# Kernel tuning notes

Hardware: AMD Instinct MI355X
Metric: run time of the kernel (lower is better)

The kernel has to match this reference:

```python
import jax, jax.numpy as jnp
import numpy as np

GROUPS = 8
EPS = 1e-3  # Keras GroupNormalization default epsilon


def group_norm(x, gamma, beta):
    b, h, w, c = x.shape
    xr = x.reshape(b, h, w, GROUPS, c // GROUPS)
    mean = jnp.mean(xr, axis=(1, 2, 4), keepdims=True)
    var = jnp.var(xr, axis=(1, 2, 4), keepdims=True)
    xn = ((xr - mean) * jax.lax.rsqrt(var + EPS)).reshape(b, h, w, c)
    return xn * gamma + beta


def setup_inputs() -> dict:
    key = jax.random.key(0)
    ks = jax.random.split(key, 6)
    B, H, W, C = 4, 64, 64, 256
    std = C ** -0.5
    return {
        "x": jax.random.normal(ks[0], (B, H, W, C), dtype=jnp.float32),
        "gamma": jnp.ones((C,), jnp.float32),
        "beta": jnp.zeros((C,), jnp.float32),
        "wq": jax.random.normal(ks[1], (C, C), jnp.float32) * std,
        "bq": jnp.zeros((C,), jnp.float32),
        "wk": jax.random.normal(ks[2], (C, C), jnp.float32) * std,
        "bk": jnp.zeros((C,), jnp.float32),
        "wv": jax.random.normal(ks[3], (C, C), jnp.float32) * std,
        "bv": jnp.zeros((C,), jnp.float32),
        "wp": jax.random.normal(ks[4], (C, C), jnp.float32) * std,
        "bp": jnp.zeros((C,), jnp.float32),
    }


def reference(x, gamma, beta, wq, bq, wk, bk, wv, bv, wp, bp):
    b, h, w, c = x.shape
    scale = jnp.asarray(c, x.dtype) ** -0.5
    xn = group_norm(x, gamma, beta)
    # 1x1 convs are per-pixel dense layers
    q = (xn @ wq + bq).reshape(b, h * w, c)
    k = (xn @ wk + bk).reshape(b, h * w, c)
    v = (xn @ wv + bv).reshape(b, h * w, c)
    scores = jnp.einsum('bic,bjc->bij', q, k) * scale  # [b, N, N]
    attn = jax.nn.softmax(scores, axis=-1)
    out = jnp.einsum('bij,bjc->bic', attn, v).reshape(b, h, w, c)
    return x + (out @ wp + bp)
```

## Files before the change

kernel.cpp:

```cpp
#include <hip/hip_runtime.h>

#define N_TOK 4096
#define C_DIM 256
#define BATCH 4
#define M_ROWS (BATCH * N_TOK)
#define GN_CNT 131072.0f
#define JSPLIT 4

typedef __attribute__((ext_vector_type(4))) float f32x4;
typedef __attribute__((ext_vector_type(16))) float f32x16;
typedef __attribute__((ext_vector_type(8))) short s16x8;
typedef __attribute__((ext_vector_type(4))) unsigned short u16x4;
typedef __attribute__((ext_vector_type(4))) unsigned int u32x4;

static __device__ __forceinline__ unsigned short f2bf(float f) {
  unsigned int u = __builtin_bit_cast(unsigned int, f);
  u += 0x7fff + ((u >> 16) & 1);
  return (unsigned short)(u >> 16);
}
static __device__ __forceinline__ float bf2f(unsigned short h) {
  unsigned int u = ((unsigned int)h) << 16;
  return __builtin_bit_cast(float, u);
}

static __device__ __forceinline__ void gload_lds16(const void* g, void* l) {
  __builtin_amdgcn_global_load_lds(
      (__attribute__((address_space(1))) void*)(unsigned long long)(const char*)g,
      (__attribute__((address_space(3))) void*)l, 16, 0, 0);
}

__global__ __launch_bounds__(256) void wtrans(const float* __restrict__ wq,
                                              const float* __restrict__ wk,
                                              const float* __restrict__ wv,
                                              const float* __restrict__ wp,
                                              unsigned short* __restrict__ wT) {
  const float* const srcs[4] = {wq, wk, wv, wp};
  const float* w = srcs[blockIdx.z];
  unsigned short* o = wT + blockIdx.z * 65536;
  __shared__ float t[32][33];
  int k0 = blockIdx.x * 32, n0 = blockIdx.y * 32;
  int tx = threadIdx.x, ty = threadIdx.y;
#pragma unroll
  for (int ky = 0; ky < 32; ky += 8)
    t[ty + ky][tx] = w[(k0 + ty + ky) * C_DIM + n0 + tx];
  __syncthreads();
#pragma unroll
  for (int ky = 0; ky < 32; ky += 8)
    o[(n0 + ty + ky) * C_DIM + k0 + tx] = f2bf(t[tx][ty + ky]);
}

__global__ __launch_bounds__(256) void gn_stats(const float* __restrict__ x,
                                                float* __restrict__ partials) {
  int bg = blockIdx.x >> 4, chunk = blockIdx.x & 15;
  int b = bg >> 3, g = bg & 7;
  int tid = threadIdx.x;
  const f32x4* x4 = (const f32x4*)x;
  float s1 = 0.f, s2 = 0.f;
#pragma unroll
  for (int it = 0; it < 8; ++it) {
    int idx = it * 256 + tid;
    int nl = idx >> 3, cq = idx & 7;
    f32x4 v = x4[(b * N_TOK + chunk * 256 + nl) * 64 + g * 8 + cq];
    s1 += v[0] + v[1] + v[2] + v[3];
    s2 += v[0] * v[0] + v[1] * v[1] + v[2] * v[2] + v[3] * v[3];
  }
  for (int m = 1; m < 64; m <<= 1) {
    s1 += __shfl_xor(s1, m, 64);
    s2 += __shfl_xor(s2, m, 64);
  }
  __shared__ float r1[4], r2[4];
  int wave = tid >> 6, lane = tid & 63;
  if (lane == 0) { r1[wave] = s1; r2[wave] = s2; }
  __syncthreads();
  if (tid == 0) {
    atomicAdd(&partials[bg * 2],     r1[0] + r1[1] + r1[2] + r1[3]);
    atomicAdd(&partials[bg * 2 + 1], r2[0] + r2[1] + r2[2] + r2[3]);
  }
}

__global__ __launch_bounds__(256, 2) void qkv_gemm(const float* __restrict__ x,
                                                   const unsigned short* __restrict__ wT,
                                                   const float* __restrict__ partials,
                                                   const float* __restrict__ gamma,
                                                   const float* __restrict__ beta,
                                                   const float* __restrict__ bq,
                                                   const float* __restrict__ bk,
                                                   const float* __restrict__ bv,
                                                   unsigned short* __restrict__ qo,
                                                   unsigned short* __restrict__ ko,
                                                   unsigned short* __restrict__ vo) {
  int tid = threadIdx.x;
  int wave = tid >> 6, lane = tid & 63, n32 = lane & 31, half = lane >> 5;
  int row0 = blockIdx.x * 128 + wave * 32;
  int w = blockIdx.y >> 1;
  int c0 = (blockIdx.y & 1) * 128;
  const unsigned short* wt = wT + w * 65536;
  __shared__ __align__(16) unsigned short Wt[32768];

#pragma unroll
  for (int ii = 0; ii < 32; ++ii) {
    int u = ii * 256 + tid;
    int n = u >> 5, ku = u & 31;
    gload_lds16(wt + (size_t)(c0 + n) * C_DIM + ((ku ^ (n & 7)) * 8), Wt + u * 8);
  }

  int row = row0 + n32;
  int batch = row >> 12;
  float mean[8], rstd[8];
  float inv = 1.f / GN_CNT;
#pragma unroll
  for (int g = 0; g < 8; ++g) {
    float m = partials[(batch * 8 + g) * 2] * inv;
    float v = partials[(batch * 8 + g) * 2 + 1] * inv - m * m;
    mean[g] = m;
    rstd[g] = rsqrtf(v + 1e-3f);
  }
  s16x8 af[16];
#pragma unroll
  for (int ks = 0; ks < 16; ++ks) {
    int cb = ks * 16 + half * 8;
    const f32x4* xp = (const f32x4*)(x + (size_t)row * C_DIM + cb);
    f32x4 v0 = xp[0], v1 = xp[1];
    const f32x4* g4 = (const f32x4*)(gamma + cb);
    const f32x4* b4 = (const f32x4*)(beta + cb);
    f32x4 ga0 = g4[0], ga1 = g4[1], be0 = b4[0], be1 = b4[1];
    int g = (2 * ks + half) >> 2;
    float m = mean[g], rs = rstd[g];
    s16x8 o;
#pragma unroll
    for (int j = 0; j < 4; ++j) {
      o[j]     = (short)f2bf((v0[j] - m) * rs * ga0[j] + be0[j]);
      o[4 + j] = (short)f2bf((v1[j] - m) * rs * ga1[j] + be1[j]);
    }
    af[ks] = o;
  }
  const float* bias = (w == 0) ? bq : (w == 1) ? bk : bv;
  unsigned short* outp = (w == 0) ? qo : (w == 1) ? ko : vo;
  float scale = (w == 0) ? 0.0625f : 1.f;
  __syncthreads();

#pragma unroll
  for (int ct = 0; ct < 4; ++ct) {
    int nl = ct * 32 + n32;
    f32x16 acc = (f32x16)(bias[c0 + nl]);
#pragma unroll
    for (int ks = 0; ks < 16; ++ks) {
      s16x8 wf = *(const s16x8*)(Wt + nl * C_DIM + (((2 * ks + half) ^ (nl & 7)) * 8));
      acc = __builtin_amdgcn_mfma_f32_32x32x16_bf16(af[ks], wf, acc, 0, 0, 0);
    }
#pragma unroll
    for (int r = 0; r < 16; ++r) {
      int rr = (r & 3) + 8 * (r >> 2) + 4 * half;
      outp[(size_t)(row0 + rr) * C_DIM + c0 + nl] = f2bf(acc[r] * scale);
    }
  }
}

__global__ __launch_bounds__(256) void vtrans(const unsigned short* __restrict__ v,
                                              unsigned short* __restrict__ vT) {
  __shared__ unsigned short t[32][33];
  int n0 = blockIdx.x * 32, c0 = blockIdx.y * 32, b = blockIdx.z;
  int tx = threadIdx.x, ty = threadIdx.y;
#pragma unroll
  for (int ky = 0; ky < 32; ky += 8)
    t[ty + ky][tx] = v[(b * N_TOK + n0 + ty + ky) * C_DIM + c0 + tx];
  __syncthreads();
#pragma unroll
  for (int ky = 0; ky < 32; ky += 8)
    vT[(b * C_DIM + c0 + ty + ky) * N_TOK + n0 + tx] = t[tx][ty + ky];
}

__global__ __launch_bounds__(256, 2) void attn_part(const unsigned short* __restrict__ q,
                                                    const unsigned short* __restrict__ k,
                                                    const unsigned short* __restrict__ vT,
                                                    unsigned short* __restrict__ op0,
                                                    unsigned short* __restrict__ op1,
                                                    unsigned short* __restrict__ op2,
                                                    unsigned short* __restrict__ op3,
                                                    float* __restrict__ lbuf) {
  int tid = threadIdx.x;
  int wave = tid >> 6, lane = tid & 63;
  int n32 = lane & 31, half = lane >> 5;
  int i = blockIdx.x;
  int batch = (i >> 1) & 3;
  int slot = ((i >> 3) << 1) | (i & 1);
  int qb = slot & 31, chunk = slot >> 5;
  int qrow0 = batch * N_TOK + qb * 128 + wave * 32;
  const unsigned short* kb = k + (size_t)batch * N_TOK * C_DIM;
  const unsigned short* vb = vT + (size_t)batch * C_DIM * N_TOK;
  unsigned short* op = (chunk == 0) ? op0 : (chunk == 1) ? op1 : (chunk == 2) ? op2 : op3;

  __shared__ __align__(16) unsigned short Kt[2][8192];
  __shared__ __align__(16) unsigned short Vt[2][8192];

  const unsigned short* qp = q + (size_t)(qrow0 + n32) * C_DIM;
  s16x8 qf[16];
#pragma unroll
  for (int ks = 0; ks < 16; ++ks)
    qf[ks] = *(const s16x8*)(qp + ks * 16 + half * 8);

  f32x16 Oa[8];
#pragma unroll
  for (int ct = 0; ct < 8; ++ct) Oa[ct] = (f32x16)(0.f);
  float ls = 0.f;
  int swz = n32 & 7;

  {
    int jbase = chunk * 1024;
#pragma unroll
    for (int ii = 0; ii < 4; ++ii) {
      int u = ii * 256 + tid;
      int tok = u >> 5, un = u & 31;
      gload_lds16(kb + (size_t)(jbase + tok) * C_DIM + ((un ^ (tok & 7)) * 8), &Kt[0][u * 8]);
    }
#pragma unroll
    for (int ii = 0; ii < 4; ++ii) {
      gload_lds16(vb + (size_t)tid * N_TOK + jbase + ii * 8, &Vt[0][(ii * 256 + tid) * 8]);
    }
  }

  int cur = 0;
  for (int jt = 0; jt < 32; ++jt) {
    __syncthreads();
    if (jt < 31) {
      int jbase = chunk * 1024 + (jt + 1) * 32;
      int nxt = cur ^ 1;
#pragma unroll
      for (int ii = 0; ii < 4; ++ii) {
        int u = ii * 256 + tid;
        int tok = u >> 5, un = u & 31;
        gload_lds16(kb + (size_t)(jbase + tok) * C_DIM + ((un ^ (tok & 7)) * 8), &Kt[nxt][u * 8]);
      }
#pragma unroll
      for (int ii = 0; ii < 4; ++ii) {
        gload_lds16(vb + (size_t)tid * N_TOK + jbase + ii * 8, &Vt[nxt][(ii * 256 + tid) * 8]);
      }
    }
    const unsigned short* KT = Kt[cur];
    const unsigned short* VT = Vt[cur];

    f32x16 sc = (f32x16)(0.f);
#pragma unroll
    for (int ks = 0; ks < 16; ++ks) {
      s16x8 kf = *(const s16x8*)(KT + n32 * 256 + (((ks * 2 + half) ^ swz) * 8));
      sc = __builtin_amdgcn_mfma_f32_32x32x16_bf16(kf, qf[ks], sc, 0, 0, 0);
    }
    unsigned D[8];
#pragma unroll
    for (int t = 0; t < 8; ++t) {
      float pa = exp2f(fmaf(sc[2 * t],     1.44269504f, -11.54156032f));
      float pb = exp2f(fmaf(sc[2 * t + 1], 1.44269504f, -11.54156032f));
      ls += pa + pb;
      D[t] = (unsigned)f2bf(pa) | ((unsigned)f2bf(pb) << 16);
    }
    unsigned E[8];
#pragma unroll
    for (int t = 0; t < 8; ++t) E[t] = __shfl_xor(D[t], 32);
    u32x4 w0 = {half ? E[2] : D[0], half ? E[3] : D[1],
                half ? D[2] : E[0], half ? D[3] : E[1]};
    u32x4 w1 = {half ? E[6] : D[4], half ? E[7] : D[5],
                half ? D[6] : E[4], half ? D[7] : E[5]};
    s16x8 pf0 = __builtin_bit_cast(s16x8, w0);
    s16x8 pf1 = __builtin_bit_cast(s16x8, w1);
#pragma unroll
    for (int ct = 0; ct < 8; ++ct) {
      int ch = ct * 32 + n32;
      s16x8 vf0 = *(const s16x8*)(VT + (half * 256 + ch) * 8);
      s16x8 vf1 = *(const s16x8*)(VT + ((2 + half) * 256 + ch) * 8);
      Oa[ct] = __builtin_amdgcn_mfma_f32_32x32x16_bf16(pf0, vf0, Oa[ct], 0, 0, 0);
      Oa[ct] = __builtin_amdgcn_mfma_f32_32x32x16_bf16(pf1, vf1, Oa[ct], 0, 0, 0);
    }
    cur ^= 1;
  }
#pragma unroll
  for (int ct = 0; ct < 8; ++ct)
#pragma unroll
    for (int r = 0; r < 16; ++r) {
      int row = (r & 3) + 8 * (r >> 2) + 4 * half;
      op[(size_t)(qrow0 + row) * C_DIM + ct * 32 + n32] = f2bf(Oa[ct][r]);
    }
  float tot = ls + __shfl_xor(ls, 32);
  if (half == 0) lbuf[chunk * M_ROWS + qrow0 + n32] = tot;
}

__global__ __launch_bounds__(256, 2) void proj_gemm(const unsigned short* __restrict__ p0,
                                                    const unsigned short* __restrict__ p1,
                                                    const unsigned short* __restrict__ p2,
                                                    const unsigned short* __restrict__ p3,
                                                    const float* __restrict__ lbuf,
                                                    const unsigned short* __restrict__ wt,
                                                    const float* __restrict__ bp,
                                                    const float* __restrict__ x,
                                                    float* __restrict__ out) {
  int tid = threadIdx.x;
  int wave = tid >> 6, lane = tid & 63, n32 = lane & 31, half = lane >> 5;
  int row0 = blockIdx.x * 128 + wave * 32;
  int c0 = blockIdx.y * 128;
  __shared__ __align__(16) unsigned short Wt[32768];

#pragma unroll
  for (int ii = 0; ii < 32; ++ii) {
    int u = ii * 256 + tid;
    int n = u >> 5, ku = u & 31;
    gload_lds16(wt + (size_t)(c0 + n) * C_DIM + ((ku ^ (n & 7)) * 8), Wt + u * 8);
  }

  int row = row0 + n32;
  float linv = 1.f / (lbuf[row] + lbuf[M_ROWS + row] +
                      lbuf[2 * M_ROWS + row] + lbuf[3 * M_ROWS + row]);
  s16x8 af[16];
#pragma unroll
  for (int ks = 0; ks < 16; ++ks) {
    size_t off = (size_t)row * C_DIM + ks * 16 + half * 8;
    s16x8 a0 = *(const s16x8*)(p0 + off);
    s16x8 a1 = *(const s16x8*)(p1 + off);
    s16x8 a2 = *(const s16x8*)(p2 + off);
    s16x8 a3 = *(const s16x8*)(p3 + off);
    s16x8 o;
#pragma unroll
    for (int j = 0; j < 8; ++j) {
      float f = bf2f((unsigned short)a0[j]) + bf2f((unsigned short)a1[j]) +
                bf2f((unsigned short)a2[j]) + bf2f((unsigned short)a3[j]);
      o[j] = (short)f2bf(f * linv);
    }
    af[ks] = o;
  }
  __syncthreads();

#pragma unroll
  for (int ct = 0; ct < 4; ++ct) {
    int nl = ct * 32 + n32;
    f32x16 acc = (f32x16)(bp[c0 + nl]);
#pragma unroll
    for (int ks = 0; ks < 16; ++ks) {
      s16x8 wf = *(const s16x8*)(Wt + nl * C_DIM + (((2 * ks + half) ^ (nl & 7)) * 8));
      acc = __builtin_amdgcn_mfma_f32_32x32x16_bf16(af[ks], wf, acc, 0, 0, 0);
    }
#pragma unroll
    for (int r = 0; r < 16; ++r) {
      int rr = (r & 3) + 8 * (r >> 2) + 4 * half;
      size_t idx = (size_t)(row0 + rr) * C_DIM + c0 + nl;
      out[idx] = acc[r] + x[idx];
    }
  }
}

extern "C" void kernel_launch(void* const* d_in, const int* in_sizes, int n_in,
                              void* d_out, int out_size, void* d_ws, size_t ws_size,
                              hipStream_t stream) {
  const float* x     = (const float*)d_in[0];
  const float* gamma = (const float*)d_in[1];
  const float* beta  = (const float*)d_in[2];
  const float* wq    = (const float*)d_in[3];
  const float* bq    = (const float*)d_in[4];
  const float* wk    = (const float*)d_in[5];
  const float* bk    = (const float*)d_in[6];
  const float* wv    = (const float*)d_in[7];
  const float* bv    = (const float*)d_in[8];
  const float* wp    = (const float*)d_in[9];
  const float* bp    = (const float*)d_in[10];
  float* out = (float*)d_out;

  char* ws = (char*)d_ws;
  const size_t MC = (size_t)M_ROWS * C_DIM;
  float* partials      = (float*)ws;
  unsigned short* wT   = (unsigned short*)(ws + 1024);
  unsigned short* qb   = wT + 4 * 65536;
  unsigned short* kbuf = qb + MC;
  unsigned short* vb   = kbuf + MC;
  unsigned short* vTb  = vb + MC;
  unsigned short* pl0  = vTb + MC;
  unsigned short* pl2  = pl0 + MC;
  unsigned short* pl3  = pl2 + MC;
  float* lbuf          = (float*)(pl3 + MC);
  unsigned short* pl1  = vb;

  hipMemsetAsync(partials, 0, 64 * sizeof(float), stream);
  wtrans<<<dim3(8, 8, 4), dim3(32, 8), 0, stream>>>(wq, wk, wv, wp, wT);
  gn_stats<<<512, 256, 0, stream>>>(x, partials);
  qkv_gemm<<<dim3(128, 6), 256, 0, stream>>>(x, wT, partials, gamma, beta,
                                             bq, bk, bv, qb, kbuf, vb);
  vtrans<<<dim3(128, 8, 4), dim3(32, 8), 0, stream>>>(vb, vTb);
  attn_part<<<512, 256, 0, stream>>>(qb, kbuf, vTb, pl0, pl1, pl2, pl3, lbuf);
  proj_gemm<<<dim3(128, 2), 256, 0, stream>>>(pl0, pl1, pl2, pl3, lbuf,
                                              wT + 3 * 65536, bp, x, out);
}
```

Before: 230.6 us.

## Merge prep kernels, drop memset and atomics, reuse normalized activations across QKV

Folds the weight transpose and group-norm statistics into one launch. Each stats block now writes its own partial-sum slot, so the memset and the atomics go away, and qkv_gemm reduces the 16 partials per group itself. qkv_gemm now normalizes each x tile once and loops over the three weight matrices, reloading each into LDS. This cuts the grid from 768 to 256 blocks, which may reduce parallelism. The attention P conversion to bf16 now truncates instead of rounding, which is cheaper but slightly less accurate.

```diff
diff --git a/kernel.cpp b/kernel.cpp
--- a/kernel.cpp
+++ b/kernel.cpp
@@ -29,52 +29,56 @@
       (__attribute__((address_space(3))) void*)l, 16, 0, 0);
 }
 
-__global__ __launch_bounds__(256) void wtrans(const float* __restrict__ wq,
-                                              const float* __restrict__ wk,
-                                              const float* __restrict__ wv,
-                                              const float* __restrict__ wp,
-                                              unsigned short* __restrict__ wT) {
-  const float* const srcs[4] = {wq, wk, wv, wp};
-  const float* w = srcs[blockIdx.z];
-  unsigned short* o = wT + blockIdx.z * 65536;
-  __shared__ float t[32][33];
-  int k0 = blockIdx.x * 32, n0 = blockIdx.y * 32;
-  int tx = threadIdx.x, ty = threadIdx.y;
-#pragma unroll
-  for (int ky = 0; ky < 32; ky += 8)
-    t[ty + ky][tx] = w[(k0 + ty + ky) * C_DIM + n0 + tx];
-  __syncthreads();
-#pragma unroll
-  for (int ky = 0; ky < 32; ky += 8)
-    o[(n0 + ty + ky) * C_DIM + k0 + tx] = f2bf(t[tx][ty + ky]);
-}
-
-__global__ __launch_bounds__(256) void gn_stats(const float* __restrict__ x,
-                                                float* __restrict__ partials) {
-  int bg = blockIdx.x >> 4, chunk = blockIdx.x & 15;
-  int b = bg >> 3, g = bg & 7;
+__global__ __launch_bounds__(256) void prep(const float* __restrict__ x,
+                                            const float* __restrict__ wq,
+                                            const float* __restrict__ wk,
+                                            const float* __restrict__ wv,
+                                            const float* __restrict__ wp,
+                                            float* __restrict__ partials,
+                                            unsigned short* __restrict__ wT) {
   int tid = threadIdx.x;
-  const f32x4* x4 = (const f32x4*)x;
-  float s1 = 0.f, s2 = 0.f;
-#pragma unroll
-  for (int it = 0; it < 8; ++it) {
-    int idx = it * 256 + tid;
-    int nl = idx >> 3, cq = idx & 7;
-    f32x4 v = x4[(b * N_TOK + chunk * 256 + nl) * 64 + g * 8 + cq];
-    s1 += v[0] + v[1] + v[2] + v[3];
-    s2 += v[0] * v[0] + v[1] * v[1] + v[2] * v[2] + v[3] * v[3];
-  }
-  for (int m = 1; m < 64; m <<= 1) {
-    s1 += __shfl_xor(s1, m, 64);
-    s2 += __shfl_xor(s2, m, 64);
-  }
-  __shared__ float r1[4], r2[4];
-  int wave = tid >> 6, lane = tid & 63;
-  if (lane == 0) { r1[wave] = s1; r2[wave] = s2; }
-  __syncthreads();
-  if (tid == 0) {
-    atomicAdd(&partials[bg * 2],     r1[0] + r1[1] + r1[2] + r1[3]);
-    atomicAdd(&partials[bg * 2 + 1], r2[0] + r2[1] + r2[2] + r2[3]);
+  if (blockIdx.x < 512) {
+    int bg = blockIdx.x >> 4, chunk = blockIdx.x & 15;
+    int b = bg >> 3, g = bg & 7;
+    const f32x4* x4 = (const f32x4*)x;
+    float s1 = 0.f, s2 = 0.f;
+#pragma unroll
+    for (int it = 0; it < 8; ++it) {
+      int idx = it * 256 + tid;
+      int nl = idx >> 3, cq = idx & 7;
+      f32x4 v = x4[(b * N_TOK + chunk * 256 + nl) * 64 + g * 8 + cq];
+      s1 += v[0] + v[1] + v[2] + v[3];
+      s2 += v[0] * v[0] + v[1] * v[1] + v[2] * v[2] + v[3] * v[3];
+    }
+    for (int m = 1; m < 64; m <<= 1) {
+      s1 += __shfl_xor(s1, m, 64);
+      s2 += __shfl_xor(s2, m, 64);
+    }
+    __shared__ float r1[4], r2[4];
+    int wave = tid >> 6, lane = tid & 63;
+    if (lane == 0) { r1[wave] = s1; r2[wave] = s2; }
+    __syncthreads();
+    if (tid == 0) {
+      int slot = (bg * 16 + chunk) * 2;
+      partials[slot]     = r1[0] + r1[1] + r1[2] + r1[3];
+      partials[slot + 1] = r2[0] + r2[1] + r2[2] + r2[3];
+    }
+  } else {
+    int rem = blockIdx.x - 512;
+    int z = rem >> 6, t = rem & 63;
+    int k0 = (t >> 3) * 32, n0 = (t & 7) * 32;
+    const float* const srcs[4] = {wq, wk, wv, wp};
+    const float* w = srcs[z];
+    unsigned short* o = wT + z * 65536;
+    __shared__ float tt[32][33];
+    int tx = tid & 31, ty = tid >> 5;
+#pragma unroll
+    for (int ky = 0; ky < 32; ky += 8)
+      tt[ty + ky][tx] = w[(k0 + ty + ky) * C_DIM + n0 + tx];
+    __syncthreads();
+#pragma unroll
+    for (int ky = 0; ky < 32; ky += 8)
+      o[(n0 + ty + ky) * C_DIM + k0 + tx] = f2bf(tt[tx][ty + ky]);
   }
 }
 
@@ -92,29 +96,33 @@
   int tid = threadIdx.x;
   int wave = tid >> 6, lane = tid & 63, n32 = lane & 31, half = lane >> 5;
   int row0 = blockIdx.x * 128 + wave * 32;
-  int w = blockIdx.y >> 1;
-  int c0 = (blockIdx.y & 1) * 128;
-  const unsigned short* wt = wT + w * 65536;
+  int c0 = blockIdx.y * 128;
+  int row = row0 + n32;
+  int batch = blockIdx.x >> 5;
   __shared__ __align__(16) unsigned short Wt[32768];
+  __shared__ float mean_s[8], rstd_s[8];
 
 #pragma unroll
   for (int ii = 0; ii < 32; ++ii) {
     int u = ii * 256 + tid;
     int n = u >> 5, ku = u & 31;
-    gload_lds16(wt + (size_t)(c0 + n) * C_DIM + ((ku ^ (n & 7)) * 8), Wt + u * 8);
-  }
-
-  int row = row0 + n32;
-  int batch = row >> 12;
+    gload_lds16(wT + (size_t)(c0 + n) * C_DIM + ((ku ^ (n & 7)) * 8), Wt + u * 8);
+  }
+  if (tid < 8) {
+    const float* p = partials + (batch * 8 + tid) * 32;
+    float s1 = 0.f, s2 = 0.f;
+#pragma unroll
+    for (int c = 0; c < 16; ++c) { s1 += p[2 * c]; s2 += p[2 * c + 1]; }
+    float inv = 1.f / GN_CNT;
+    float m = s1 * inv, v = s2 * inv - m * m;
+    mean_s[tid] = m;
+    rstd_s[tid] = rsqrtf(v + 1e-3f);
+  }
+  __syncthreads();
+
   float mean[8], rstd[8];
-  float inv = 1.f / GN_CNT;
-#pragma unroll
-  for (int g = 0; g < 8; ++g) {
-    float m = partials[(batch * 8 + g) * 2] * inv;
-    float v = partials[(batch * 8 + g) * 2 + 1] * inv - m * m;
-    mean[g] = m;
-    rstd[g] = rsqrtf(v + 1e-3f);
-  }
+#pragma unroll
+  for (int g = 0; g < 8; ++g) { mean[g] = mean_s[g]; rstd[g] = rstd_s[g]; }
   s16x8 af[16];
 #pragma unroll
   for (int ks = 0; ks < 16; ++ks) {
@@ -134,24 +142,36 @@
     }
     af[ks] = o;
   }
-  const float* bias = (w == 0) ? bq : (w == 1) ? bk : bv;
-  unsigned short* outp = (w == 0) ? qo : (w == 1) ? ko : vo;
-  float scale = (w == 0) ? 0.0625f : 1.f;
-  __syncthreads();
-
-#pragma unroll
-  for (int ct = 0; ct < 4; ++ct) {
-    int nl = ct * 32 + n32;
-    f32x16 acc = (f32x16)(bias[c0 + nl]);
-#pragma unroll
-    for (int ks = 0; ks < 16; ++ks) {
-      s16x8 wf = *(const s16x8*)(Wt + nl * C_DIM + (((2 * ks + half) ^ (nl & 7)) * 8));
-      acc = __builtin_amdgcn_mfma_f32_32x32x16_bf16(af[ks], wf, acc, 0, 0, 0);
-    }
-#pragma unroll
-    for (int r = 0; r < 16; ++r) {
-      int rr = (r & 3) + 8 * (r >> 2) + 4 * half;
-      outp[(size_t)(row0 + rr) * C_DIM + c0 + nl] = f2bf(acc[r] * scale);
+
+  for (int w = 0; w < 3; ++w) {
+    if (w > 0) {
+      __syncthreads();
+#pragma unroll
+      for (int ii = 0; ii < 32; ++ii) {
+        int u = ii * 256 + tid;
+        int n = u >> 5, ku = u & 31;
+        gload_lds16(wT + (size_t)w * 65536 + (size_t)(c0 + n) * C_DIM + ((ku ^ (n & 7)) * 8),
+                    Wt + u * 8);
+      }
+      __syncthreads();
+    }
+    const float* bias = (w == 0) ? bq : (w == 1) ? bk : bv;
+    unsigned short* outp = (w == 0) ? qo : (w == 1) ? ko : vo;
+    float scale = (w == 0) ? 0.0625f : 1.f;
+#pragma unroll
+    for (int ct = 0; ct < 4; ++ct) {
+      int nl = ct * 32 + n32;
+      f32x16 acc = (f32x16)(bias[c0 + nl]);
+#pragma unroll
+      for (int ks = 0; ks < 16; ++ks) {
+        s16x8 wf = *(const s16x8*)(Wt + nl * C_DIM + (((2 * ks + half) ^ (nl & 7)) * 8));
+        acc = __builtin_amdgcn_mfma_f32_32x32x16_bf16(af[ks], wf, acc, 0, 0, 0);
+      }
+#pragma unroll
+      for (int r = 0; r < 16; ++r) {
+        int rr = (r & 3) + 8 * (r >> 2) + 4 * half;
+        outp[(size_t)(row0 + rr) * C_DIM + c0 + nl] = f2bf(acc[r] * scale);
+      }
     }
   }
 }
@@ -251,7 +271,8 @@
       float pa = exp2f(fmaf(sc[2 * t],     1.44269504f, -11.54156032f));
       float pb = exp2f(fmaf(sc[2 * t + 1], 1.44269504f, -11.54156032f));
       ls += pa + pb;
-      D[t] = (unsigned)f2bf(pa) | ((unsigned)f2bf(pb) << 16);
+      D[t] = (__builtin_bit_cast(unsigned, pa) >> 16) |
+             (__builtin_bit_cast(unsigned, pb) & 0xFFFF0000u);
     }
     unsigned E[8];
 #pragma unroll
@@ -364,7 +385,7 @@
   char* ws = (char*)d_ws;
   const size_t MC = (size_t)M_ROWS * C_DIM;
   float* partials      = (float*)ws;
-  unsigned short* wT   = (unsigned short*)(ws + 1024);
+  unsigned short* wT   = (unsigned short*)(ws + 4096);
   unsigned short* qb   = wT + 4 * 65536;
   unsigned short* kbuf = qb + MC;
   unsigned short* vb   = kbuf + MC;
@@ -375,10 +396,8 @@
   float* lbuf          = (float*)(pl3 + MC);
   unsigned short* pl1  = vb;
 
-  hipMemsetAsync(partials, 0, 64 * sizeof(float), stream);
-  wtrans<<<dim3(8, 8, 4), dim3(32, 8), 0, stream>>>(wq, wk, wv, wp, wT);
-  gn_stats<<<512, 256, 0, stream>>>(x, partials);
-  qkv_gemm<<<dim3(128, 6), 256, 0, stream>>>(x, wT, partials, gamma, beta,
+  prep<<<768, 256, 0, stream>>>(x, wq, wk, wv, wp, partials, wT);
+  qkv_gemm<<<dim3(128, 2), 256, 0, stream>>>(x, wT, partials, gamma, beta,
                                              bq, bk, bv, qb, kbuf, vb);
   vtrans<<<dim3(128, 8, 4), dim3(32, 8), 0, stream>>>(vb, vTb);
   attn_part<<<512, 256, 0, stream>>>(qb, kbuf, vTb, pl0, pl1, pl2, pl3, lbuf);
```

Measured after the change: 223.5 us. -3.1%, faster.
